# Optimization experiments

Measured on AMD Instinct MI355X. Metric: run time of the kernel, lower is better.

## Reference

```python
import jax, jax.numpy as jnp
import numpy as np

INPUT_SIZE = 128
OUTPUT_SIZE = 128
P_NUM = 16
BATCH = 131072


def setup_inputs() -> dict:
    key = jax.random.key(0)
    k_x, k_c = jax.random.split(key)
    x = jax.random.normal(k_x, (BATCH, INPUT_SIZE), dtype=jnp.float32)
    coef = jax.random.normal(k_c, (OUTPUT_SIZE, INPUT_SIZE, P_NUM), dtype=jnp.float32) * 0.1
    tanh_range = jnp.array(1.0, dtype=jnp.float32)
    return {"x": x, "coef": coef, "tanh_range": tanh_range}


def reference(x, coef, tanh_range):
    # Original: values = tanh(x*t); out[b,o] = sum_i sum_p coef[o,i,p] * values[b,i]
    # Equivalent fused form: (sum_p coef) applied as a single GEMM.
    values = jnp.tanh(x * tanh_range)          # [B, I]
    w = jnp.sum(coef, axis=2)                  # [O, I]
    return jnp.einsum('bi,oi->bo', values, w)  # [B, O]
```

## Files before the change

kernel.cpp:

```cpp
#include <hip/hip_runtime.h>

#define BATCH 131072
#define IN 128
#define OUT 128
#define PNUM 16
#define LDS_PITCH 136

typedef _Float16 f16x8 __attribute__((ext_vector_type(8)));
typedef float f32x4 __attribute__((ext_vector_type(4)));

__device__ __forceinline__ float tanh_fast(float v) {
    float e = __expf(2.0f * v);
    return 1.0f - 2.0f * __builtin_amdgcn_rcpf(e + 1.0f);
}

__global__ __launch_bounds__(256) void prep_w_kernel(const float* __restrict__ coef,
                                                     _Float16* __restrict__ w) {
    int t = blockIdx.x * blockDim.x + threadIdx.x;
    const float4* p = (const float4*)(coef + (size_t)t * PNUM);
    float4 a = p[0], b = p[1], c = p[2], d = p[3];
    float s = (a.x + a.y + a.z + a.w) + (b.x + b.y + b.z + b.w)
            + (c.x + c.y + c.z + c.w) + (d.x + d.y + d.z + d.w);
    w[t] = (_Float16)s;
}

__global__ __launch_bounds__(512, 5) void gemm_tanh_kernel(const float* __restrict__ x,
                                                           const _Float16* __restrict__ w,
                                                           const float* __restrict__ trange,
                                                           float* __restrict__ out) {
    __shared__ _Float16 wlds[OUT * LDS_PITCH];

    const float t = trange[0];
    const int tid  = threadIdx.x;
    const int lane = tid & 63;
    const int wv   = tid >> 6;
    const int m = lane & 15;
    const int q = lane >> 4;

    const size_t row_base = (size_t)blockIdx.x * 128 + (size_t)wv * 16;
    const float* xrow = x + (row_base + m) * IN;

    float4 xv[8];
#pragma unroll
    for (int ks = 0; ks < 4; ++ks) {
        xv[2 * ks]     = *(const float4*)(xrow + ks * 32 + q * 8);
        xv[2 * ks + 1] = *(const float4*)(xrow + ks * 32 + q * 8 + 4);
    }

#pragma unroll
    for (int i = 0; i < 4; ++i) {
        int idx = (i * 512 + tid) * 8;
        int r = idx >> 7;
        int c = idx & 127;
        *(f16x8*)&wlds[r * LDS_PITCH + c] = *(const f16x8*)(w + idx);
    }
    __syncthreads();

    f16x8 af[4];
#pragma unroll
    for (int ks = 0; ks < 4; ++ks) {
        float4 a = xv[2 * ks], b = xv[2 * ks + 1];
        af[ks][0] = (_Float16)tanh_fast(a.x * t);
        af[ks][1] = (_Float16)tanh_fast(a.y * t);
        af[ks][2] = (_Float16)tanh_fast(a.z * t);
        af[ks][3] = (_Float16)tanh_fast(a.w * t);
        af[ks][4] = (_Float16)tanh_fast(b.x * t);
        af[ks][5] = (_Float16)tanh_fast(b.y * t);
        af[ks][6] = (_Float16)tanh_fast(b.z * t);
        af[ks][7] = (_Float16)tanh_fast(b.w * t);
    }

    f32x4 acc[8];
#pragma unroll
    for (int nt = 0; nt < 8; ++nt) acc[nt] = (f32x4){0.f, 0.f, 0.f, 0.f};

#pragma unroll
    for (int ks = 0; ks < 4; ++ks) {
        const int kb = ks * 32 + q * 8;
#pragma unroll
        for (int nt = 0; nt < 8; ++nt) {
            f16x8 bf = *(const f16x8*)&wlds[(nt * 16 + m) * LDS_PITCH + kb];
            acc[nt] = __builtin_amdgcn_mfma_f32_16x16x32_f16(af[ks], bf, acc[nt], 0, 0, 0);
        }
    }

    float* orow = out + (row_base + q * 4) * OUT + m;
#pragma unroll
    for (int nt = 0; nt < 8; ++nt) {
#pragma unroll
        for (int r = 0; r < 4; ++r) {
            orow[(size_t)r * OUT + nt * 16] = acc[nt][r];
        }
    }
}

extern "C" void kernel_launch(void* const* d_in, const int* in_sizes, int n_in,
                              void* d_out, int out_size, void* d_ws, size_t ws_size,
                              hipStream_t stream) {
    const float* x    = (const float*)d_in[0];
    const float* coef = (const float*)d_in[1];
    const float* tr   = (const float*)d_in[2];
    float* out = (float*)d_out;
    _Float16* w = (_Float16*)d_ws;

    prep_w_kernel<<<(OUT * IN) / 256, 256, 0, stream>>>(coef, w);
    gemm_tanh_kernel<<<BATCH / 128, 512, 0, stream>>>(x, w, tr, out);
}
```

Measured before the change: 119.3 us.

## Transpose MFMA operands for vectorized output stores, add nontemporal loads/stores

Swaps the A/B operands of the MFMA so each lane holds four consecutive output columns, which lets the epilogue write 16-byte vector nontemporal stores in place of scattered scalar stores. Input loads are made nontemporal, tanh is rewritten with exp2 and a prescaled constant plus an fma, and the weight buffer moves into a device global in place of the workspace. Occupancy hint drops from 5 to 4 waves per SIMD. The main target is store coalescing on a bandwidth-bound kernel; the nontemporal hints and the lower occupancy hint may affect cache behaviour and latency hiding.

```diff
diff --git a/kernel.cpp b/kernel.cpp
--- a/kernel.cpp
+++ b/kernel.cpp
@@ -9,28 +9,23 @@
 typedef _Float16 f16x8 __attribute__((ext_vector_type(8)));
 typedef float f32x4 __attribute__((ext_vector_type(4)));
 
-__device__ __forceinline__ float tanh_fast(float v) {
-    float e = __expf(2.0f * v);
-    return 1.0f - 2.0f * __builtin_amdgcn_rcpf(e + 1.0f);
-}
+__device__ _Float16 g_w[OUT * IN];
 
-__global__ __launch_bounds__(256) void prep_w_kernel(const float* __restrict__ coef,
-                                                     _Float16* __restrict__ w) {
+__global__ __launch_bounds__(256) void prep_w_kernel(const float* __restrict__ coef) {
     int t = blockIdx.x * blockDim.x + threadIdx.x;
     const float4* p = (const float4*)(coef + (size_t)t * PNUM);
     float4 a = p[0], b = p[1], c = p[2], d = p[3];
     float s = (a.x + a.y + a.z + a.w) + (b.x + b.y + b.z + b.w)
             + (c.x + c.y + c.z + c.w) + (d.x + d.y + d.z + d.w);
-    w[t] = (_Float16)s;
+    g_w[t] = (_Float16)s;
 }
 
-__global__ __launch_bounds__(512, 5) void gemm_tanh_kernel(const float* __restrict__ x,
-                                                           const _Float16* __restrict__ w,
+__global__ __launch_bounds__(512, 4) void gemm_tanh_kernel(const float* __restrict__ x,
                                                            const float* __restrict__ trange,
                                                            float* __restrict__ out) {
     __shared__ _Float16 wlds[OUT * LDS_PITCH];
 
-    const float t = trange[0];
+    const float ts = trange[0] * 2.8853900817779268f;
     const int tid  = threadIdx.x;
     const int lane = tid & 63;
     const int wv   = tid >> 6;
@@ -40,11 +35,13 @@
     const size_t row_base = (size_t)blockIdx.x * 128 + (size_t)wv * 16;
     const float* xrow = x + (row_base + m) * IN;
 
-    float4 xv[8];
+    f32x4 xv[8];
 #pragma unroll
     for (int ks = 0; ks < 4; ++ks) {
-        xv[2 * ks]     = *(const float4*)(xrow + ks * 32 + q * 8);
-        xv[2 * ks + 1] = *(const float4*)(xrow + ks * 32 + q * 8 + 4);
+        xv[2 * ks]     = __builtin_nontemporal_load(
+            reinterpret_cast<const f32x4*>(xrow + ks * 32 + q * 8));
+        xv[2 * ks + 1] = __builtin_nontemporal_load(
+            reinterpret_cast<const f32x4*>(xrow + ks * 32 + q * 8 + 4));
     }
 
 #pragma unroll
@@ -52,22 +49,21 @@
         int idx = (i * 512 + tid) * 8;
         int r = idx >> 7;
         int c = idx & 127;
-        *(f16x8*)&wlds[r * LDS_PITCH + c] = *(const f16x8*)(w + idx);
+        *(f16x8*)&wlds[r * LDS_PITCH + c] = *(const f16x8*)(g_w + idx);
     }
     __syncthreads();
 
     f16x8 af[4];
 #pragma unroll
     for (int ks = 0; ks < 4; ++ks) {
-        float4 a = xv[2 * ks], b = xv[2 * ks + 1];
-        af[ks][0] = (_Float16)tanh_fast(a.x * t);
-        af[ks][1] = (_Float16)tanh_fast(a.y * t);
-        af[ks][2] = (_Float16)tanh_fast(a.z * t);
-        af[ks][3] = (_Float16)tanh_fast(a.w * t);
-        af[ks][4] = (_Float16)tanh_fast(b.x * t);
-        af[ks][5] = (_Float16)tanh_fast(b.y * t);
-        af[ks][6] = (_Float16)tanh_fast(b.z * t);
-        af[ks][7] = (_Float16)tanh_fast(b.w * t);
+        f32x4 a = xv[2 * ks], b = xv[2 * ks + 1];
+#pragma unroll
+        for (int e = 0; e < 4; ++e) {
+            float ea = __builtin_amdgcn_exp2f(a[e] * ts);
+            float eb = __builtin_amdgcn_exp2f(b[e] * ts);
+            af[ks][e]     = (_Float16)__builtin_fmaf(-2.0f, __builtin_amdgcn_rcpf(ea + 1.0f), 1.0f);
+            af[ks][e + 4] = (_Float16)__builtin_fmaf(-2.0f, __builtin_amdgcn_rcpf(eb + 1.0f), 1.0f);
+        }
     }
 
     f32x4 acc[8];
@@ -80,17 +76,14 @@
 #pragma unroll
         for (int nt = 0; nt < 8; ++nt) {
             f16x8 bf = *(const f16x8*)&wlds[(nt * 16 + m) * LDS_PITCH + kb];
-            acc[nt] = __builtin_amdgcn_mfma_f32_16x16x32_f16(af[ks], bf, acc[nt], 0, 0, 0);
+            acc[nt] = __builtin_amdgcn_mfma_f32_16x16x32_f16(bf, af[ks], acc[nt], 0, 0, 0);
         }
     }
 
-    float* orow = out + (row_base + q * 4) * OUT + m;
+    float* orow = out + (row_base + m) * OUT + q * 4;
 #pragma unroll
     for (int nt = 0; nt < 8; ++nt) {
-#pragma unroll
-        for (int r = 0; r < 4; ++r) {
-            orow[(size_t)r * OUT + nt * 16] = acc[nt][r];
-        }
+        __builtin_nontemporal_store(acc[nt], reinterpret_cast<f32x4*>(orow + nt * 16));
     }
 }
 
@@ -101,8 +94,8 @@
     const float* coef = (const float*)d_in[1];
     const float* tr   = (const float*)d_in[2];
     float* out = (float*)d_out;
-    _Float16* w = (_Float16*)d_ws;
+    (void)d_ws; (void)ws_size;
 
-    prep_w_kernel<<<(OUT * IN) / 256, 256, 0, stream>>>(coef, w);
-    gemm_tanh_kernel<<<BATCH / 128, 512, 0, stream>>>(x, w, tr, out);
+    prep_w_kernel<<<(OUT * IN) / 256, 256, 0, stream>>>(coef);
+    gemm_tanh_kernel<<<BATCH / 128, 512, 0, stream>>>(x, tr, out);
 }
```

After: 128.5 us. +7.7%, slower.
